# Performance work log

Hardware: AMD Instinct MI355X
Metric: run time of the kernel (lower is better)

The kernel has to match this reference:

```python
import jax, jax.numpy as jnp
import numpy as np
import math

DIM = 2048
N_HEADS = 16
HEAD_DIM = 128
BATCH = 2
T = 2048
EPS = 1e-5


def setup_inputs() -> dict:
    key = jax.random.key(0)
    ks = jax.random.split(key, 16)
    s = lambda fan_in: 1.0 / math.sqrt(fan_in)
    d = {}
    d['x'] = jax.random.normal(ks[0], (BATCH, T, DIM), dtype=jnp.float32)
    d['start_pos'] = 0
    # attention projections (weights stored [in, out])
    d['wq'] = jax.random.uniform(ks[1], (DIM, N_HEADS * HEAD_DIM), minval=-s(DIM), maxval=s(DIM))
    d['bq'] = jnp.zeros((N_HEADS * HEAD_DIM,), jnp.float32)
    d['wk'] = jax.random.uniform(ks[2], (DIM, HEAD_DIM), minval=-s(DIM), maxval=s(DIM))
    d['bk'] = jnp.zeros((HEAD_DIM,), jnp.float32)
    d['wv'] = jax.random.uniform(ks[3], (DIM, HEAD_DIM), minval=-s(DIM), maxval=s(DIM))
    d['bv'] = jnp.zeros((HEAD_DIM,), jnp.float32)
    d['wo'] = jax.random.uniform(ks[4], (N_HEADS * HEAD_DIM, DIM), minval=-s(N_HEADS * HEAD_DIM), maxval=s(N_HEADS * HEAD_DIM))
    d['bo'] = jnp.zeros((DIM,), jnp.float32)
    # layernorms
    d['ln1_g'] = jnp.ones((DIM,), jnp.float32)
    d['ln1_b'] = jnp.zeros((DIM,), jnp.float32)
    d['ln2_g'] = jnp.ones((DIM,), jnp.float32)
    d['ln2_b'] = jnp.zeros((DIM,), jnp.float32)
    # MLP (dim -> 4*dim -> dim), dropout p=0 is a no-op
    d['w1'] = jax.random.uniform(ks[5], (DIM, 4 * DIM), minval=-s(DIM), maxval=s(DIM))
    d['b1'] = jnp.zeros((4 * DIM,), jnp.float32)
    d['w2'] = jax.random.uniform(ks[6], (4 * DIM, DIM), minval=-s(4 * DIM), maxval=s(4 * DIM))
    d['b2'] = jnp.zeros((DIM,), jnp.float32)
    return d


def _layernorm(h, g, b):
    mu = jnp.mean(h, axis=-1, keepdims=True)
    var = jnp.mean(jnp.square(h - mu), axis=-1, keepdims=True)
    return (h - mu) * jax.lax.rsqrt(var + EPS) * g + b


def reference(x, start_pos, wq, bq, wk, bk, wv, bv, wo, bo, ln1_g, ln1_b, ln2_g, ln2_b, w1, b1, w2, b2):
    B, Tq, D = x.shape
    hd = wk.shape[1]
    H = wq.shape[1] // hd
    # --- MQA attention on pre-LN input (prefill: no kv cache) ---
    h = _layernorm(x, ln1_g, ln1_b)
    q = (h @ wq + bq).reshape(B, Tq, H, hd)          # [B,T,H,hd]
    k = h @ wk + bk                                   # [B,T,hd] single shared head
    v = h @ wv + bv                                   # [B,T,hd]
    scores = jnp.einsum('bthc,bsc->bhts', q, k) / math.sqrt(hd)
    causal = jnp.where(jnp.tril(jnp.ones((Tq, Tq), dtype=bool)), 0.0, -jnp.inf).astype(scores.dtype)
    attn = jax.nn.softmax(scores + causal, axis=-1)   # [B,H,T,T]
    ctx = jnp.einsum('bhts,bsc->bthc', attn, v).reshape(B, Tq, H * hd)
    out = ctx @ wo + bo
    x = x + out
    # --- GELU MLP (exact erf gelu, torch default) ---
    h2 = _layernorm(x, ln2_g, ln2_b)
    x = x + jax.nn.gelu(h2 @ w1 + b1, approximate=False) @ w2 + b2
    k_cat = k[:, None]                                # [B,1,T,hd]
    v_cat = v[:, None]
    return (x, k_cat, v_cat)
```

## Files before the change

### kernel.cpp

```cpp
#include <hip/hip_runtime.h>
#include <stdint.h>

#define DIMSZ 2048
#define HD 128
#define NH 16
#define BATCH 2
#define SEQ 2048
#define MROWS (BATCH*SEQ)
#define FFDIM (4*DIMSZ)
#define NQKV (DIMSZ + 2*HD)

typedef float f32x4 __attribute__((ext_vector_type(4)));
typedef __bf16 bf16x8 __attribute__((ext_vector_type(8)));
typedef __bf16 bf16x2 __attribute__((ext_vector_type(2)));
typedef __bf16 bf16_t;

__device__ __forceinline__ void async16(const void* g, void* l) {
  __builtin_amdgcn_global_load_lds(
      (const __attribute__((address_space(1))) void*)(uintptr_t)g,
      (__attribute__((address_space(3))) void*)(uint32_t)(uintptr_t)l,
      16, 0, 0);
}

__device__ __forceinline__ float gelu_f(float x) {
  return 0.5f * x * (1.0f + erff(x * 0.70710678118654752f));
}

__device__ __forceinline__ void hard_barrier() {
  asm volatile("" ::: "memory");
  __builtin_amdgcn_s_barrier();
  asm volatile("" ::: "memory");
}

__global__ __launch_bounds__(256)
void k_tr64(const float* __restrict__ src, bf16_t* __restrict__ dst,
            int R, int C) {
  __shared__ float tile[64][65];
  int c0 = blockIdx.x * 64, r0 = blockIdx.y * 64;
  int lc = threadIdx.x & 63, lrow = threadIdx.x >> 6;
#pragma unroll
  for (int i = 0; i < 64; i += 4)
    tile[lrow + i][lc] = src[(size_t)(r0 + lrow + i) * C + c0 + lc];
  __syncthreads();
  int rp = threadIdx.x & 31, wc = threadIdx.x >> 5;
#pragma unroll
  for (int i = 0; i < 64; i += 8) {
    int c = wc + i;
    bf16x2 pk = {(bf16_t)tile[2 * rp][c], (bf16_t)tile[2 * rp + 1][c]};
    *(bf16x2*)(dst + (size_t)(c0 + c) * R + r0 + 2 * rp) = pk;
  }
}

__global__ __launch_bounds__(256)
void k_transpose_v(const bf16_t* __restrict__ v, bf16_t* __restrict__ vt) {
  __shared__ bf16_t tile[32][33];
  int b = blockIdx.z;
  int t0 = blockIdx.x * 32, d0 = blockIdx.y * 32;
  int tx = threadIdx.x & 31, ty = threadIdx.x >> 5;
#pragma unroll
  for (int i = 0; i < 32; i += 8)
    tile[ty + i][tx] = v[((size_t)(b * SEQ + t0 + ty + i)) * HD + d0 + tx];
  __syncthreads();
#pragma unroll
  for (int i = 0; i < 32; i += 8)
    vt[((size_t)(b * HD + d0 + ty + i)) * SEQ + t0 + tx] = tile[tx][ty + i];
}

__global__ __launch_bounds__(256)
void k_layernorm(const float* __restrict__ x, const float* __restrict__ g,
                 const float* __restrict__ bb, bf16_t* __restrict__ out) {
  int row = blockIdx.x;
  const float* xr = x + (size_t)row * DIMSZ;
  int t = threadIdx.x;
  float vals[8];
  float s = 0.f, s2 = 0.f;
#pragma unroll
  for (int i = 0; i < 8; ++i) {
    float v = xr[t + i * 256];
    vals[i] = v; s += v; s2 += v * v;
  }
#pragma unroll
  for (int o = 1; o < 64; o <<= 1) { s += __shfl_xor(s, o); s2 += __shfl_xor(s2, o); }
  __shared__ float red[8];
  if ((t & 63) == 0) { red[t >> 6] = s; red[4 + (t >> 6)] = s2; }
  __syncthreads();
  s = red[0] + red[1] + red[2] + red[3];
  s2 = red[4] + red[5] + red[6] + red[7];
  float mu = s * (1.0f / DIMSZ);
  float rstd = rsqrtf(s2 * (1.0f / DIMSZ) - mu * mu + 1e-5f);
  bf16_t* orow = out + (size_t)row * DIMSZ;
#pragma unroll
  for (int i = 0; i < 8; ++i) {
    int c = t + i * 256;
    orow[c] = (bf16_t)((vals[i] - mu) * rstd * g[c] + bb[c]);
  }
}

template <int FN>
__device__ __forceinline__ void gemm8_loop(
    const bf16_t* __restrict__ A, const bf16_t* __restrict__ BT,
    int ld, int Kloop, int bm, int bn, f32x4 (&acc)[8][FN], bf16_t* sh) {
  constexpr int BH = FN >> 1;
  constexpr int BN = FN * 64;
  const int tid = threadIdx.x;
  const int lane = tid & 63, lr = lane & 15, lg = lane >> 4;
  const int wave = tid >> 6, wm = wave >> 2, wn = wave & 3;
  bf16_t* const Ab0 = sh;
  bf16_t* const Bb0 = sh + 32768;
  const bf16_t* const Ag = A + (size_t)bm * 256 * ld;
  const bf16_t* const Bg = BT + (size_t)bn * BN * ld;

  auto stage = [&](const bf16_t* gbase, bf16_t* lbase, int h, int t) {
#pragma unroll
    for (int j = 0; j < 2; ++j) {
      int flat = (tid + j * 512) * 8;
      int r = flat >> 6, kp = flat & 63;
      int ks = kp ^ ((r & 7) << 3);
      async16(gbase + (size_t)(h * 128 + r) * ld + t * 64 + ks, lbase + flat);
    }
  };
  auto stA = [&](int c, int h, int t) { stage(Ag, Ab0 + (c * 2 + h) * 8192, h, t); };
  auto stB = [&](int c, int h, int t) { stage(Bg, Bb0 + (c * BH + h) * 8192, h, t); };

  const int xsw = (lr & 7) << 3;
  bf16x8 a_[8], b_[FN][2];
  auto lda = [&](int c, int kk) {
    const bf16_t* base = Ab0 + (c * 2 + wm) * 8192;
#pragma unroll
    for (int mf = 0; mf < 8; ++mf)
      a_[mf] = *(const bf16x8*)(base + (mf * 16 + lr) * 64 + ((kk + lg * 8) ^ xsw));
  };
  auto ldb = [&](int c) {
#pragma unroll
    for (int nf = 0; nf < FN; ++nf) {
      int row = wn * (FN * 16) + nf * 16 + lr;
      const bf16_t* base =
          Bb0 + (c * BH + (BH == 2 ? (row >> 7) : 0)) * 8192 + (row & 127) * 64;
#pragma unroll
      for (int kx = 0; kx < 2; ++kx)
        b_[nf][kx] = *(const bf16x8*)(base + ((kx * 32 + lg * 8) ^ xsw));
    }
  };

#define LGKM0 asm volatile("s_waitcnt lgkmcnt(0)" ::: "memory");
#define VMC_STEADY                                                   \
  if (BH == 2) { asm volatile("s_waitcnt vmcnt(6)" ::: "memory"); }  \
  else         { asm volatile("s_waitcnt vmcnt(4)" ::: "memory"); }
#define MFMA_HALF(M0, KX)                                            \
  __builtin_amdgcn_s_setprio(1);                                     \
  _Pragma("unroll")                                                  \
  for (int mf = 0; mf < 4; ++mf)                                     \
    _Pragma("unroll")                                                \
    for (int nf = 0; nf < FN; ++nf)                                  \
      acc[(M0) + mf][nf] = __builtin_amdgcn_mfma_f32_16x16x32_bf16(  \
          a_[(M0) + mf], b_[nf][KX], acc[(M0) + mf][nf], 0, 0, 0);   \
  __builtin_amdgcn_s_setprio(0);

  const int nit = Kloop >> 7;

  stA(0, 0, 0); stA(0, 1, 0);
  stB(0, 0, 0); if (BH == 2) stB(0, 1, 0);
  stB(1, 0, 1); if (BH == 2) stB(1, 1, 1);
  stA(1, 0, 1);
  VMC_STEADY;
  hard_barrier();

  for (int i = 0; i < nit; ++i) {
    const int t1 = 2 * i + 1, t2 = 2 * i + 2, t3 = 2 * i + 3;
    const bool g2 = (i < nit - 1);
    lda(0, 0); ldb(0);
    stA(1, 1, t1);
    hard_barrier(); LGKM0;
    MFMA_HALF(0, 0)
    hard_barrier();
    if (g2) stB(0, 0, t2);
    hard_barrier();
    MFMA_HALF(4, 0)
    hard_barrier();
    lda(0, 32);
    if (g2 && BH == 2) stB(0, 1, t2);
    hard_barrier(); LGKM0;
    MFMA_HALF(0, 1)
    hard_barrier();
    if (g2) stA(0, 0, t2);
    if (i == nit - 1) { asm volatile("s_waitcnt vmcnt(0)" ::: "memory"); }
    else { VMC_STEADY; }
    hard_barrier();
    MFMA_HALF(4, 1)
    hard_barrier();
    lda(1, 0); ldb(1);
    if (g2) stA(0, 1, t2);
    hard_barrier(); LGKM0;
    MFMA_HALF(0, 0)
    hard_barrier();
    if (g2) stB(1, 0, t3);
    hard_barrier();
    MFMA_HALF(4, 0)
    hard_barrier();
    lda(1, 32);
    if (g2 && BH == 2) stB(1, 1, t3);
    hard_barrier(); LGKM0;
    MFMA_HALF(0, 1)
    hard_barrier();
    if (g2) {
      stA(1, 0, t3);
      VMC_STEADY;
    }
    hard_barrier();
    MFMA_HALF(4, 1)
    hard_barrier();
  }
#undef LGKM0
#undef VMC_STEADY
#undef MFMA_HALF
}

__global__ __launch_bounds__(512, 1)
void k_oproj(const bf16_t* __restrict__ A, const bf16_t* __restrict__ BT,
             const float* __restrict__ bias, const float* __restrict__ res,
             float* __restrict__ outF) {
  extern __shared__ __align__(16) bf16_t sh8[];
  const int nt = DIMSZ / 128;
  int bm = blockIdx.x / nt, bn = blockIdx.x % nt;
  f32x4 acc[8][2] = {};
  gemm8_loop<2>(A, BT, DIMSZ, DIMSZ, bm, bn, acc, sh8);
  int tid = threadIdx.x, wave = tid >> 6, lane = tid & 63, lr = lane & 15, lg = lane >> 4;
  int wm = wave >> 2, wn = wave & 3;
  float* shF = (float*)sh8;
  int rl0 = wm * 128 + lg * 4;
  int cl0 = wn * 32 + lr;
#pragma unroll
  for (int nf = 0; nf < 2; ++nf) {
    int cl = cl0 + nf * 16;
    float bi = bias[bn * 128 + cl];
#pragma unroll
    for (int mf = 0; mf < 8; ++mf)
#pragma unroll
      for (int j = 0; j < 4; ++j)
        shF[(rl0 + mf * 16 + j) * 128 + cl] = acc[mf][nf][j] + bi;
  }
  hard_barrier();
  const float* rbase = res + (size_t)(bm * 256) * DIMSZ + bn * 128;
  float* gbase = outF + (size_t)(bm * 256) * DIMSZ + bn * 128;
#pragma unroll
  for (int s = 0; s < 16; ++s) {
    int flat = s * 512 + tid;
    int row = flat >> 5, cu = flat & 31;
    f32x4 v = *(const f32x4*)(shF + row * 128 + cu * 4);
    f32x4 r4 = *(const f32x4*)(rbase + (size_t)row * DIMSZ + cu * 4);
    *(f32x4*)(gbase + (size_t)row * DIMSZ + cu * 4) = v + r4;
  }
}

__global__ __launch_bounds__(512, 1)
void k_ffn1(const bf16_t* __restrict__ A, const bf16_t* __restrict__ BT,
            const float* __restrict__ bias, bf16_t* __restrict__ outB) {
  extern __shared__ __align__(16) bf16_t sh8[];
  const int nt = FFDIM / 256;
  int bm = blockIdx.x / nt, bn = blockIdx.x % nt;
  f32x4 acc[8][4] = {};
  gemm8_loop<4>(A, BT, DIMSZ, DIMSZ, bm, bn, acc, sh8);
  int tid = threadIdx.x, wave = tid >> 6, lane = tid & 63, lr = lane & 15, lg = lane >> 4;
  int wm = wave >> 2, wn = wave & 3;
  int rl0 = wm * 128 + lg * 4;
  int cl0 = wn * 64 + lr;
#pragma unroll
  for (int nf = 0; nf < 4; ++nf) {
    int cl = cl0 + nf * 16;
    float bi = bias[bn * 256 + cl];
#pragma unroll
    for (int mf = 0; mf < 8; ++mf)
#pragma unroll
      for (int j = 0; j < 4; ++j)
        sh8[(rl0 + mf * 16 + j) * 256 + cl] = (bf16_t)gelu_f(acc[mf][nf][j] + bi);
  }
  hard_barrier();
  bf16_t* gbase = outB + (size_t)(bm * 256) * FFDIM + bn * 256;
#pragma unroll
  for (int s = 0; s < 16; ++s) {
    int flat = s * 512 + tid;
    int row = flat >> 5, cu = flat & 31;
    f32x4 v = *(const f32x4*)(sh8 + row * 256 + cu * 8);
    *(f32x4*)(gbase + (size_t)row * FFDIM + cu * 8) = v;
  }
}

__global__ __launch_bounds__(512, 1)
void k_ffn2(const bf16_t* __restrict__ A, const bf16_t* __restrict__ BT,
            const float* __restrict__ bias, float* __restrict__ outF) {
  extern __shared__ __align__(16) bf16_t sh8[];
  int swz = (blockIdx.x & 7) * 32 + (blockIdx.x >> 3);
  int kh = swz >> 7;
  int tile = swz & 127;
  int bm = tile >> 3, bn = tile & 7;
  f32x4 acc[8][4] = {};
  gemm8_loop<4>(A + kh * (FFDIM / 2), BT + kh * (FFDIM / 2), FFDIM, FFDIM / 2,
                bm, bn, acc, sh8);
  int tid = threadIdx.x, wave = tid >> 6, lane = tid & 63, lr = lane & 15, lg = lane >> 4;
  int wm = wave >> 2, wn = wave & 3;
  int row0 = bm * 256 + wm * 128 + lg * 4;
  int col0 = bn * 256 + wn * 64 + lr;
#pragma unroll
  for (int nf = 0; nf < 4; ++nf) {
    int c = col0 + nf * 16;
    float bi = kh ? 0.f : bias[c];
#pragma unroll
    for (int mf = 0; mf < 8; ++mf)
#pragma unroll
      for (int j = 0; j < 4; ++j) {
        int r = row0 + mf * 16 + j;
        __hip_atomic_fetch_add(&outF[(size_t)r * DIMSZ + c], acc[mf][nf][j] + bi,
                               __ATOMIC_RELAXED, __HIP_MEMORY_SCOPE_AGENT);
      }
  }
}

__global__ __launch_bounds__(512, 1)
void k_qkv(const bf16_t* __restrict__ A, const bf16_t* __restrict__ BT,
           const float* __restrict__ bq, const float* __restrict__ bk,
           const float* __restrict__ bv,
           bf16_t* __restrict__ qb, float* __restrict__ outk,
           float* __restrict__ outv, bf16_t* __restrict__ kbf,
           bf16_t* __restrict__ vbf) {
  extern __shared__ __align__(16) bf16_t sh8[];
  const int nt = NQKV / 256;
  int bm = blockIdx.x / nt, bn = blockIdx.x % nt;
  f32x4 acc[8][4] = {};
  gemm8_loop<4>(A, BT, DIMSZ, DIMSZ, bm, bn, acc, sh8);
  int tid = threadIdx.x, wave = tid >> 6, lane = tid & 63, lr = lane & 15, lg = lane >> 4;
  int wm = wave >> 2, wn = wave & 3;
  int rl0 = wm * 128 + lg * 4;
  int cl0 = wn * 64 + lr;
#pragma unroll
  for (int nf = 0; nf < 4; ++nf) {
    int cl = cl0 + nf * 16;
    int cg = bn * 256 + cl;
    float bi = (cg < 2048) ? bq[cg] : (cg < 2176 ? bk[cg - 2048] : bv[cg - 2176]);
#pragma unroll
    for (int mf = 0; mf < 8; ++mf)
#pragma unroll
      for (int j = 0; j < 4; ++j) {
        float v = acc[mf][nf][j] + bi;
        sh8[(rl0 + mf * 16 + j) * 256 + cl] = (bf16_t)v;
        if (cg >= 2048) {
          int r = bm * 256 + rl0 + mf * 16 + j;
          if (cg < 2176) outk[(size_t)r * HD + (cg - 2048)] = v;
          else           outv[(size_t)r * HD + (cg - 2176)] = v;
        }
      }
  }
  hard_barrier();
#pragma unroll
  for (int s = 0; s < 16; ++s) {
    int flat = s * 512 + tid;
    int row = flat >> 5, cu = flat & 31;
    f32x4 v = *(const f32x4*)(sh8 + row * 256 + cu * 8);
    int r = bm * 256 + row;
    if (bn < 8) {
      *(f32x4*)(qb + (size_t)r * DIMSZ + bn * 256 + cu * 8) = v;
    } else {
      int ce = cu * 8;
      if (ce < 128) *(f32x4*)(kbf + (size_t)r * HD + ce) = v;
      else          *(f32x4*)(vbf + (size_t)r * HD + (ce - 128)) = v;
    }
  }
}

__global__ __launch_bounds__(256, 2)
void k_attn(const bf16_t* __restrict__ q, const bf16_t* __restrict__ k,
            const bf16_t* __restrict__ vt, bf16_t* __restrict__ ctx) {
  __shared__ __align__(16) bf16_t Ks[2][64 * 128];
  __shared__ __align__(16) bf16_t Vs[2][128 * 64];
  __shared__ bf16_t Pw[4][16][72];
  int pp = blockIdx.x, h = blockIdx.y, b = blockIdx.z;
  int tid = threadIdx.x, wave = tid >> 6, lane = tid & 63, lr = lane & 15, lg = lane >> 4;
  const bf16_t* kb = k + (size_t)b * SEQ * HD;
  const bf16_t* vb = vt + (size_t)b * HD * SEQ;

#define STAGE_TILE(buf, s0_)                                                      \
  {                                                                               \
    _Pragma("unroll")                                                             \
    for (int i = 0; i < 4; ++i) {                                                 \
      int flat = (i * 256 + tid) * 8;                                             \
      int kr = flat >> 7, kc = flat & 127;                                        \
      int ksrc = (((kc >> 3) ^ (kr & 7)) << 3) | (kc & 7);                        \
      async16(kb + (size_t)((s0_) + kr) * HD + ksrc, (void*)(Ks[buf] + flat));    \
      int vr = flat >> 6, vc = flat & 63;                                         \
      int vsrc = (((vc >> 3) ^ (vr & 7)) << 3) | (vc & 7);                        \
      async16(vb + (size_t)vr * SEQ + (s0_) + vsrc, (void*)(Vs[buf] + flat));     \
    }                                                                             \
  }

  for (int half = 0; half < 2; ++half) {
    int qt = half ? (31 - pp) : pp;
    int q0 = qt * 64;
    int qw = q0 + wave * 16;
    const bf16_t* qbase = q + ((size_t)(b * SEQ + qw + lr)) * DIMSZ + h * HD;
    bf16x8 qf[4];
#pragma unroll
    for (int kk = 0; kk < 4; ++kk) qf[kk] = *(const bf16x8*)(qbase + kk * 32 + lg * 8);
    f32x4 o[8] = {};
    float m_[4], l_[4];
#pragma unroll
    for (int j = 0; j < 4; ++j) { m_[j] = -3.0e38f; l_[j] = 0.f; }
    int qglob0 = qw + lg * 4;
    int ntiles = qt + 1;

    STAGE_TILE(0, 0)
    __syncthreads();
    for (int t = 0; t < ntiles; ++t) {
      int cur = t & 1;
      if (t + 1 < ntiles) STAGE_TILE(cur ^ 1, (t + 1) * 64)
      int s0 = t * 64;
      const bf16_t* Kc = Ks[cur];
      const bf16_t* Vc = Vs[cur];
      f32x4 sf[4] = {};
#pragma unroll
      for (int nf = 0; nf < 4; ++nf) {
        int R = nf * 16 + lr;
#pragma unroll
        for (int kk = 0; kk < 4; ++kk)
          sf[nf] = __builtin_amdgcn_mfma_f32_16x16x32_bf16(
              qf[kk],
              *(const bf16x8*)(Kc + R * 128 + (((kk * 4 + lg) ^ (R & 7)) << 3)),
              sf[nf], 0, 0, 0);
      }
#pragma unroll
      for (int nf = 0; nf < 4; ++nf) {
        int col = s0 + nf * 16 + lr;
#pragma unroll
        for (int j = 0; j < 4; ++j) {
          float v = sf[nf][j] * 0.088388347648318447f;
          sf[nf][j] = (col <= qglob0 + j) ? v : -3.0e38f;
        }
      }
      float mx[4];
#pragma unroll
      for (int j = 0; j < 4; ++j)
        mx[j] = fmaxf(fmaxf(sf[0][j], sf[1][j]), fmaxf(sf[2][j], sf[3][j]));
#pragma unroll
      for (int o_ = 1; o_ < 16; o_ <<= 1)
#pragma unroll
        for (int j = 0; j < 4; ++j) mx[j] = fmaxf(mx[j], __shfl_xor(mx[j], o_));
      float fsc[4], mn[4];
#pragma unroll
      for (int j = 0; j < 4; ++j) {
        mn[j] = fmaxf(m_[j], mx[j]);
        fsc[j] = __expf(m_[j] - mn[j]);
        m_[j] = mn[j];
      }
      float ps[4] = {0.f, 0.f, 0.f, 0.f};
#pragma unroll
      for (int nf = 0; nf < 4; ++nf)
#pragma unroll
        for (int j = 0; j < 4; ++j) {
          float pv = __expf(sf[nf][j] - mn[j]);
          ps[j] += pv;
          Pw[wave][lg * 4 + j][nf * 16 + lr] = (bf16_t)pv;
        }
#pragma unroll
      for (int o_ = 1; o_ < 16; o_ <<= 1)
#pragma unroll
        for (int j = 0; j < 4; ++j) ps[j] += __shfl_xor(ps[j], o_);
#pragma unroll
      for (int j = 0; j < 4; ++j) l_[j] = l_[j] * fsc[j] + ps[j];
#pragma unroll
      for (int df = 0; df < 8; ++df)
#pragma unroll
        for (int j = 0; j < 4; ++j) o[df][j] *= fsc[j];
      asm volatile("" ::: "memory");
      bf16x8 pa[2];
#pragma unroll
      for (int kk = 0; kk < 2; ++kk)
        pa[kk] = *(const bf16x8*)(&Pw[wave][lr][kk * 32 + lg * 8]);
#pragma unroll
      for (int df = 0; df < 8; ++df) {
        int R = df * 16 + lr;
#pragma unroll
        for (int kk = 0; kk < 2; ++kk)
          o[df] = __builtin_amdgcn_mfma_f32_16x16x32_bf16(
              pa[kk],
              *(const bf16x8*)(Vc + R * 64 + (((kk * 4 + lg) ^ (R & 7)) << 3)),
              o[df], 0, 0, 0);
      }
      __syncthreads();
    }
    bf16_t* cb = ctx + ((size_t)(b * SEQ + qw)) * DIMSZ + h * HD;
#pragma unroll
    for (int df = 0; df < 8; ++df)
#pragma unroll
      for (int j = 0; j < 4; ++j)
        cb[(size_t)(lg * 4 + j) * DIMSZ + df * 16 + lr] = (bf16_t)(o[df][j] / l_[j]);
  }
#undef STAGE_TILE
}

extern "C" void kernel_launch(void* const* d_in, const int* in_sizes, int n_in,
                              void* d_out, int out_size, void* d_ws, size_t ws_size,
                              hipStream_t stream) {
  const float* x   = (const float*)d_in[0];
  const float* wq  = (const float*)d_in[2];
  const float* bq  = (const float*)d_in[3];
  const float* wk  = (const float*)d_in[4];
  const float* bk  = (const float*)d_in[5];
  const float* wv  = (const float*)d_in[6];
  const float* bv  = (const float*)d_in[7];
  const float* wo  = (const float*)d_in[8];
  const float* bo  = (const float*)d_in[9];
  const float* g1  = (const float*)d_in[10];
  const float* be1 = (const float*)d_in[11];
  const float* g2  = (const float*)d_in[12];
  const float* be2 = (const float*)d_in[13];
  const float* w1  = (const float*)d_in[14];
  const float* bb1 = (const float*)d_in[15];
  const float* w2  = (const float*)d_in[16];
  const float* bb2 = (const float*)d_in[17];

  float* outx = (float*)d_out;
  float* outk = outx + (size_t)MROWS * DIMSZ;
  float* outv = outk + (size_t)MROWS * HD;

  char* p = (char*)d_ws;
  auto alloc = [&](size_t bytes) -> char* {
    char* r = p;
    p += (bytes + 255) & ~(size_t)255;
    return r;
  };
  bf16_t* wqkvT = (bf16_t*)alloc((size_t)NQKV * DIMSZ * 2);
  bf16_t* woT = (bf16_t*)alloc((size_t)DIMSZ * DIMSZ * 2);
  bf16_t* w1T = (bf16_t*)alloc((size_t)FFDIM * DIMSZ * 2);
  bf16_t* w2T = (bf16_t*)alloc((size_t)DIMSZ * FFDIM * 2);
  bf16_t* hb  = (bf16_t*)alloc((size_t)MROWS * DIMSZ * 2);
  bf16_t* qb  = (bf16_t*)alloc((size_t)MROWS * DIMSZ * 2);
  bf16_t* kbf = (bf16_t*)alloc((size_t)MROWS * HD * 2);
  bf16_t* vbf = (bf16_t*)alloc((size_t)MROWS * HD * 2);
  bf16_t* vtb = (bf16_t*)alloc((size_t)BATCH * HD * SEQ * 2);
  bf16_t* f1b = (bf16_t*)alloc((size_t)MROWS * FFDIM * 2);
  (void)ws_size; (void)in_sizes; (void)n_in; (void)out_size;

  dim3 blk(256);
  const int LDSG = 131072;
  k_tr64<<<dim3(DIMSZ / 64, DIMSZ / 64), blk, 0, stream>>>(wq, wqkvT, DIMSZ, DIMSZ);
  k_tr64<<<dim3(HD / 64, DIMSZ / 64), blk, 0, stream>>>(wk, wqkvT + (size_t)2048 * DIMSZ, DIMSZ, HD);
  k_tr64<<<dim3(HD / 64, DIMSZ / 64), blk, 0, stream>>>(wv, wqkvT + (size_t)2176 * DIMSZ, DIMSZ, HD);
  k_tr64<<<dim3(DIMSZ / 64, DIMSZ / 64), blk, 0, stream>>>(wo, woT, DIMSZ, DIMSZ);
  k_tr64<<<dim3(FFDIM / 64, DIMSZ / 64), blk, 0, stream>>>(w1, w1T, DIMSZ, FFDIM);
  k_tr64<<<dim3(DIMSZ / 64, FFDIM / 64), blk, 0, stream>>>(w2, w2T, FFDIM, DIMSZ);
  k_layernorm<<<MROWS, blk, 0, stream>>>(x, g1, be1, hb);
  k_qkv<<<(MROWS / 256) * (NQKV / 256), 512, LDSG, stream>>>(
      hb, wqkvT, bq, bk, bv, qb, outk, outv, kbf, vbf);
  k_transpose_v<<<dim3(SEQ / 32, HD / 32, BATCH), blk, 0, stream>>>(vbf, vtb);
  k_attn<<<dim3(SEQ / 64 / 2, NH, BATCH), blk, 0, stream>>>(qb, kbf, vtb, hb);
  k_oproj<<<(MROWS / 256) * (DIMSZ / 128), 512, LDSG, stream>>>(hb, woT, bo, x, outx);
  k_layernorm<<<MROWS, blk, 0, stream>>>(outx, g2, be2, qb);
  k_ffn1<<<(MROWS / 256) * (FFDIM / 256), 512, LDSG, stream>>>(qb, w1T, bb1, f1b);
  k_ffn2<<<256, 512, LDSG, stream>>>(f1b, w2T, bb2, outx);
}
```

Measured before the change: 554.3 us.

## Replace FFN2 split-K atomics with fp16 partial buffers plus reduction kernel

The FFN2 split-K GEMM now writes each K-half's partial tile as fp16 into separate workspace buffers through LDS with coalesced 16-byte stores. A new reduction kernel then adds both partials, the bias and the residual into the output. This removes per-element fp32 atomic adds to global memory. The six weight-transpose launches are also merged into one kernel. Storing partials in fp16 loses precision and adds an extra pass over memory.

```diff
diff --git a/kernel.cpp b/kernel.cpp
--- a/kernel.cpp
+++ b/kernel.cpp
@@ -13,7 +13,9 @@
 typedef float f32x4 __attribute__((ext_vector_type(4)));
 typedef __bf16 bf16x8 __attribute__((ext_vector_type(8)));
 typedef __bf16 bf16x2 __attribute__((ext_vector_type(2)));
+typedef _Float16 f16x8 __attribute__((ext_vector_type(8)));
 typedef __bf16 bf16_t;
+typedef _Float16 f16_t;
 
 __device__ __forceinline__ void async16(const void* g, void* l) {
   __builtin_amdgcn_global_load_lds(
@@ -33,10 +35,22 @@
 }
 
 __global__ __launch_bounds__(256)
-void k_tr64(const float* __restrict__ src, bf16_t* __restrict__ dst,
-            int R, int C) {
+void k_trall(const float* __restrict__ wq, const float* __restrict__ wk,
+             const float* __restrict__ wv, const float* __restrict__ wo,
+             const float* __restrict__ w1, const float* __restrict__ w2,
+             bf16_t* __restrict__ wqkvT, bf16_t* __restrict__ woT,
+             bf16_t* __restrict__ w1T, bf16_t* __restrict__ w2T) {
+  int bid = blockIdx.x;
+  const float* src; bf16_t* dst; int R, C, t0;
+  if (bid < 1024)      { src = wq; dst = wqkvT;                        R = 2048; C = 2048; t0 = bid; }
+  else if (bid < 1088) { src = wk; dst = wqkvT + (size_t)2048 * 2048;  R = 2048; C = 128;  t0 = bid - 1024; }
+  else if (bid < 1152) { src = wv; dst = wqkvT + (size_t)2176 * 2048;  R = 2048; C = 128;  t0 = bid - 1088; }
+  else if (bid < 2176) { src = wo; dst = woT;                          R = 2048; C = 2048; t0 = bid - 1152; }
+  else if (bid < 6272) { src = w1; dst = w1T;                          R = 2048; C = 8192; t0 = bid - 2176; }
+  else                 { src = w2; dst = w2T;                          R = 8192; C = 2048; t0 = bid - 6272; }
+  int tc = C >> 6;
+  int c0 = (t0 % tc) * 64, r0 = (t0 / tc) * 64;
   __shared__ float tile[64][65];
-  int c0 = blockIdx.x * 64, r0 = blockIdx.y * 64;
   int lc = threadIdx.x & 63, lrow = threadIdx.x >> 6;
 #pragma unroll
   for (int i = 0; i < 64; i += 4)
@@ -287,7 +301,7 @@
 
 __global__ __launch_bounds__(512, 1)
 void k_ffn2(const bf16_t* __restrict__ A, const bf16_t* __restrict__ BT,
-            const float* __restrict__ bias, float* __restrict__ outF) {
+            f16_t* __restrict__ p0, f16_t* __restrict__ p1) {
   extern __shared__ __align__(16) bf16_t sh8[];
   int swz = (blockIdx.x & 7) * 32 + (blockIdx.x >> 3);
   int kh = swz >> 7;
@@ -298,21 +312,48 @@
                 bm, bn, acc, sh8);
   int tid = threadIdx.x, wave = tid >> 6, lane = tid & 63, lr = lane & 15, lg = lane >> 4;
   int wm = wave >> 2, wn = wave & 3;
-  int row0 = bm * 256 + wm * 128 + lg * 4;
-  int col0 = bn * 256 + wn * 64 + lr;
+  f16_t* shH = (f16_t*)sh8;
+  int rl0 = wm * 128 + lg * 4;
+  int cl0 = wn * 64 + lr;
 #pragma unroll
   for (int nf = 0; nf < 4; ++nf) {
-    int c = col0 + nf * 16;
-    float bi = kh ? 0.f : bias[c];
+    int cl = cl0 + nf * 16;
 #pragma unroll
     for (int mf = 0; mf < 8; ++mf)
 #pragma unroll
-      for (int j = 0; j < 4; ++j) {
-        int r = row0 + mf * 16 + j;
-        __hip_atomic_fetch_add(&outF[(size_t)r * DIMSZ + c], acc[mf][nf][j] + bi,
-                               __ATOMIC_RELAXED, __HIP_MEMORY_SCOPE_AGENT);
-      }
-  }
+      for (int j = 0; j < 4; ++j)
+        shH[(rl0 + mf * 16 + j) * 256 + cl] = (f16_t)acc[mf][nf][j];
+  }
+  hard_barrier();
+  f16_t* gbase = (kh ? p1 : p0) + (size_t)(bm * 256) * DIMSZ + bn * 256;
+#pragma unroll
+  for (int s = 0; s < 16; ++s) {
+    int flat = s * 512 + tid;
+    int row = flat >> 5, cu = flat & 31;
+    f32x4 v = *(const f32x4*)(shH + row * 256 + cu * 8);
+    *(f32x4*)(gbase + (size_t)row * DIMSZ + cu * 8) = v;
+  }
+}
+
+__global__ __launch_bounds__(256)
+void k_ffn2red(const f16_t* __restrict__ p0, const f16_t* __restrict__ p1,
+               const float* __restrict__ b2, float* __restrict__ outx) {
+  int row = blockIdx.x;
+  int c0 = threadIdx.x * 8;
+  size_t base = (size_t)row * DIMSZ + c0;
+  f16x8 a = *(const f16x8*)(p0 + base);
+  f16x8 b = *(const f16x8*)(p1 + base);
+  f32x4 o0 = *(const f32x4*)(outx + base);
+  f32x4 o1 = *(const f32x4*)(outx + base + 4);
+  f32x4 b0 = *(const f32x4*)(b2 + c0);
+  f32x4 b1 = *(const f32x4*)(b2 + c0 + 4);
+#pragma unroll
+  for (int i = 0; i < 4; ++i) {
+    o0[i] += (float)a[i] + (float)b[i] + b0[i];
+    o1[i] += (float)a[4 + i] + (float)b[4 + i] + b1[i];
+  }
+  *(f32x4*)(outx + base) = o0;
+  *(f32x4*)(outx + base + 4) = o1;
 }
 
 __global__ __launch_bounds__(512, 1)
@@ -536,16 +577,13 @@
   bf16_t* vbf = (bf16_t*)alloc((size_t)MROWS * HD * 2);
   bf16_t* vtb = (bf16_t*)alloc((size_t)BATCH * HD * SEQ * 2);
   bf16_t* f1b = (bf16_t*)alloc((size_t)MROWS * FFDIM * 2);
+  f16_t* p0  = (f16_t*)alloc((size_t)MROWS * DIMSZ * 2);
+  f16_t* p1  = (f16_t*)alloc((size_t)MROWS * DIMSZ * 2);
   (void)ws_size; (void)in_sizes; (void)n_in; (void)out_size;
 
   dim3 blk(256);
   const int LDSG = 131072;
-  k_tr64<<<dim3(DIMSZ / 64, DIMSZ / 64), blk, 0, stream>>>(wq, wqkvT, DIMSZ, DIMSZ);
-  k_tr64<<<dim3(HD / 64, DIMSZ / 64), blk, 0, stream>>>(wk, wqkvT + (size_t)2048 * DIMSZ, DIMSZ, HD);
-  k_tr64<<<dim3(HD / 64, DIMSZ / 64), blk, 0, stream>>>(wv, wqkvT + (size_t)2176 * DIMSZ, DIMSZ, HD);
-  k_tr64<<<dim3(DIMSZ / 64, DIMSZ / 64), blk, 0, stream>>>(wo, woT, DIMSZ, DIMSZ);
-  k_tr64<<<dim3(FFDIM / 64, DIMSZ / 64), blk, 0, stream>>>(w1, w1T, DIMSZ, FFDIM);
-  k_tr64<<<dim3(DIMSZ / 64, FFDIM / 64), blk, 0, stream>>>(w2, w2T, FFDIM, DIMSZ);
+  k_trall<<<10368, blk, 0, stream>>>(wq, wk, wv, wo, w1, w2, wqkvT, woT, w1T, w2T);
   k_layernorm<<<MROWS, blk, 0, stream>>>(x, g1, be1, hb);
   k_qkv<<<(MROWS / 256) * (NQKV / 256), 512, LDSG, stream>>>(
       hb, wqkvT, bq, bk, bv, qb, outk, outv, kbf, vbf);
@@ -554,5 +592,6 @@
   k_oproj<<<(MROWS / 256) * (DIMSZ / 128), 512, LDSG, stream>>>(hb, woT, bo, x, outx);
   k_layernorm<<<MROWS, blk, 0, stream>>>(outx, g2, be2, qb);
   k_ffn1<<<(MROWS / 256) * (FFDIM / 256), 512, LDSG, stream>>>(qb, w1T, bb1, f1b);
-  k_ffn2<<<256, 512, LDSG, stream>>>(f1b, w2T, bb2, outx);
-}
+  k_ffn2<<<256, 512, LDSG, stream>>>(f1b, w2T, p0, p1);
+  k_ffn2red<<<MROWS, blk, 0, stream>>>(p0, p1, bb2, outx);
+}
```

Result: faster. 523.0 us, median of 3 (-5.6%).
